# Performance work log

Hardware: AMD Instinct MI355X
Metric: run time of the kernel (lower is better)

The kernel has to match this reference:

```python
import jax, jax.numpy as jnp
import numpy as np

VOCAB = 32000
EMB_DIM = 2048
N_COMP = 64   # number of component token sequences (len(input_ids))
SEQ_L = 128   # tokens per component
BATCH = 4096  # rows of input_ratio


def setup_inputs() -> dict:
    key = jax.random.key(0)
    k1, k2, k3 = jax.random.split(key, 3)
    input_ids = jax.random.randint(k1, (N_COMP, SEQ_L), 0, VOCAB)
    input_ratio = jax.random.uniform(k2, (BATCH, N_COMP), dtype=jnp.float32)
    emb_weight = jax.random.normal(k3, (VOCAB, EMB_DIM), dtype=jnp.float32)
    return {"input_ids": input_ids, "input_ratio": input_ratio, "emb_weight": emb_weight}


def reference(input_ids, input_ratio, emb_weight):
    # Per-component embedding gather + mean pool over tokens: [N, L, D] -> [N, D]
    pooled = jnp.mean(emb_weight[input_ids], axis=1)
    # Ratio mixing: [B, N] @ [N, D] -> [B, D]
    return jnp.matmul(input_ratio, pooled)
```

## Files before the change

### kernel.cpp

```cpp
#include <hip/hip_runtime.h>

#define VOCAB   32000
#define EMB_DIM 2048
#define N_COMP  64
#define SEQ_L   128
#define BATCH   4096

__global__ __launch_bounds__(256) void gather_sum(
    const int* __restrict__ ids,
    const float* __restrict__ emb,
    float* __restrict__ S) {
  const int n   = blockIdx.x;
  const int col = blockIdx.y * 1024 + threadIdx.x * 4;
  const int t0  = blockIdx.z * 32;

  float4 acc = make_float4(0.f, 0.f, 0.f, 0.f);
  const int* idp = ids + n * SEQ_L + t0;

#pragma unroll 8
  for (int t = 0; t < 32; ++t) {
    const int id = idp[t];
    const float4 v = *(const float4*)(emb + (size_t)id * EMB_DIM + col);
    acc.x += v.x; acc.y += v.y; acc.z += v.z; acc.w += v.w;
  }

  float* o = S + n * EMB_DIM + col;
  atomicAdd(o + 0, acc.x);
  atomicAdd(o + 1, acc.y);
  atomicAdd(o + 2, acc.z);
  atomicAdd(o + 3, acc.w);
}

__global__ __launch_bounds__(256) void mix(
    const float* __restrict__ ratio,
    const float* __restrict__ S,
    float* __restrict__ out) {
  const int row0 = blockIdx.x * 16;
  const int col  = blockIdx.y * 1024 + threadIdx.x * 4;

  float4 acc[16];
#pragma unroll
  for (int r = 0; r < 16; ++r) acc[r] = make_float4(0.f, 0.f, 0.f, 0.f);

#pragma unroll 4
  for (int n = 0; n < N_COMP; ++n) {
    const float4 p = *(const float4*)(S + n * EMB_DIM + col);
#pragma unroll
    for (int r = 0; r < 16; ++r) {
      const float s = ratio[(row0 + r) * N_COMP + n];
      acc[r].x += s * p.x;
      acc[r].y += s * p.y;
      acc[r].z += s * p.z;
      acc[r].w += s * p.w;
    }
  }

  const float inv = 1.0f / (float)SEQ_L;
#pragma unroll
  for (int r = 0; r < 16; ++r) {
    float4 o;
    o.x = acc[r].x * inv; o.y = acc[r].y * inv;
    o.z = acc[r].z * inv; o.w = acc[r].w * inv;
    *(float4*)(out + (size_t)(row0 + r) * EMB_DIM + col) = o;
  }
}

extern "C" void kernel_launch(void* const* d_in, const int* in_sizes, int n_in,
                              void* d_out, int out_size, void* d_ws, size_t ws_size,
                              hipStream_t stream) {
  const int*   ids   = (const int*)d_in[0];
  const float* ratio = (const float*)d_in[1];
  const float* emb   = (const float*)d_in[2];
  float* out = (float*)d_out;
  float* S   = (float*)d_ws;

  hipMemsetAsync(S, 0, (size_t)N_COMP * EMB_DIM * sizeof(float), stream);

  gather_sum<<<dim3(N_COMP, 2, 4), 256, 0, stream>>>(ids, emb, S);
  mix<<<dim3(BATCH / 16, 2), 256, 0, stream>>>(ratio, S, out);
}
```

Baseline: 341.1 us.

## Replace atomic gather accumulation with in-block shared-memory reduction and drop memset

```diff
diff --git a/kernel.cpp b/kernel.cpp
--- a/kernel.cpp
+++ b/kernel.cpp
@@ -6,29 +6,33 @@
 #define SEQ_L   128
 #define BATCH   4096
 
-__global__ __launch_bounds__(256) void gather_sum(
+__global__ __launch_bounds__(256) void gather_pool(
     const int* __restrict__ ids,
     const float* __restrict__ emb,
     float* __restrict__ S) {
-  const int n   = blockIdx.x;
-  const int col = blockIdx.y * 1024 + threadIdx.x * 4;
-  const int t0  = blockIdx.z * 32;
+  const int n     = blockIdx.x;
+  const int chunk = blockIdx.y;
+  const int tid   = threadIdx.x;
+  const int w     = tid >> 6;
+  const int lane  = tid & 63;
+  const int col   = chunk * 256 + lane * 4;
+
+  const int* idp = ids + n * SEQ_L + w * 32;
 
   float4 acc = make_float4(0.f, 0.f, 0.f, 0.f);
-  const int* idp = ids + n * SEQ_L + t0;
-
-#pragma unroll 8
+#pragma unroll
   for (int t = 0; t < 32; ++t) {
     const int id = idp[t];
     const float4 v = *(const float4*)(emb + (size_t)id * EMB_DIM + col);
     acc.x += v.x; acc.y += v.y; acc.z += v.z; acc.w += v.w;
   }
 
-  float* o = S + n * EMB_DIM + col;
-  atomicAdd(o + 0, acc.x);
-  atomicAdd(o + 1, acc.y);
-  atomicAdd(o + 2, acc.z);
-  atomicAdd(o + 3, acc.w);
+  __shared__ float red[4 * 256];
+  *(float4*)(red + w * 256 + lane * 4) = acc;
+  __syncthreads();
+
+  const float s = red[tid] + red[256 + tid] + red[512 + tid] + red[768 + tid];
+  S[n * EMB_DIM + chunk * 256 + tid] = s * (1.0f / (float)SEQ_L);
 }
 
 __global__ __launch_bounds__(256) void mix(
@@ -42,7 +46,7 @@
 #pragma unroll
   for (int r = 0; r < 16; ++r) acc[r] = make_float4(0.f, 0.f, 0.f, 0.f);
 
-#pragma unroll 4
+#pragma unroll 8
   for (int n = 0; n < N_COMP; ++n) {
     const float4 p = *(const float4*)(S + n * EMB_DIM + col);
 #pragma unroll
@@ -55,13 +59,9 @@
     }
   }
 
-  const float inv = 1.0f / (float)SEQ_L;
 #pragma unroll
   for (int r = 0; r < 16; ++r) {
-    float4 o;
-    o.x = acc[r].x * inv; o.y = acc[r].y * inv;
-    o.z = acc[r].z * inv; o.w = acc[r].w * inv;
-    *(float4*)(out + (size_t)(row0 + r) * EMB_DIM + col) = o;
+    *(float4*)(out + (size_t)(row0 + r) * EMB_DIM + col) = acc[r];
   }
 }
 
@@ -74,8 +74,6 @@
   float* out = (float*)d_out;
   float* S   = (float*)d_ws;
 
-  hipMemsetAsync(S, 0, (size_t)N_COMP * EMB_DIM * sizeof(float), stream);
-
-  gather_sum<<<dim3(N_COMP, 2, 4), 256, 0, stream>>>(ids, emb, S);
+  gather_pool<<<dim3(N_COMP, EMB_DIM / 256), 256, 0, stream>>>(ids, emb, S);
   mix<<<dim3(BATCH / 16, 2), 256, 0, stream>>>(ratio, S, out);
 }
```

Result: faster. 331.2 us (-2.9%).
